# Kernel tuning notes

Hardware: AMD Instinct MI355X
Metric: run time of the kernel (lower is better)

The kernel has to match this reference:

```python
import jax, jax.numpy as jnp
import numpy as np

N = 100000
E = 1600000
IN_FEATS = 256
OUT_FEATS = 256
EPS_WSUM = 1e-8   # clamp for weight sum
EPS_NORM = 1e-12  # F.normalize eps


def setup_inputs() -> dict:
    key = jax.random.key(0)
    k1, k2, k3, k4, k5 = jax.random.split(key, 5)
    x = jax.random.normal(k1, (N, IN_FEATS), dtype=jnp.float32)
    edge_index = jax.random.randint(k2, (2, E), 0, N, dtype=jnp.int64)
    edge_weight = jax.random.uniform(k3, (E,), dtype=jnp.float32)
    # Xavier-uniform-like init scale for [out, in] weights
    lim = float(np.sqrt(6.0 / (IN_FEATS + OUT_FEATS)) * np.sqrt(2.0))
    W_self = jax.random.uniform(k4, (OUT_FEATS, IN_FEATS), dtype=jnp.float32, minval=-lim, maxval=lim)
    W_neigh = jax.random.uniform(k5, (OUT_FEATS, IN_FEATS), dtype=jnp.float32, minval=-lim, maxval=lim)
    bias = jnp.zeros((OUT_FEATS,), dtype=jnp.float32)
    return {"x": x, "edge_index": edge_index, "edge_weight": edge_weight,
            "W_self": W_self, "W_neigh": W_neigh, "bias": bias}


def reference(x, edge_index, edge_weight, W_self, W_neigh, bias):
    row, col = edge_index[0], edge_index[1]
    # weighted mean aggregation: gather -> scale -> scatter-add -> normalize by weight sum
    weighted = x[row] * edge_weight[:, None]                       # [E, in]
    num = jax.ops.segment_sum(weighted, col, num_segments=N)       # [N, in]
    wsum = jax.ops.segment_sum(edge_weight, col, num_segments=N)   # [N]
    wsum = jnp.maximum(wsum, EPS_WSUM)
    neigh = num / wsum[:, None]                                    # [N, in]
    out = x @ W_self.T + neigh @ W_neigh.T + bias                  # [N, out]
    # L2 normalize (torch F.normalize semantics)
    nrm = jnp.maximum(jnp.linalg.norm(out, axis=-1, keepdims=True), EPS_NORM)
    return out / nrm
```

## Files before the change

kernel.cpp:

```cpp
#include <hip/hip_runtime.h>
#include <hip/hip_bf16.h>
#include <stdint.h>

#define IN_F 256
#define K_TOT 512
#define GR 64

typedef __attribute__((ext_vector_type(8))) _Float16 f16x8;
typedef __attribute__((ext_vector_type(4))) _Float16 f16x4;
typedef __attribute__((ext_vector_type(4))) float f32x4;
typedef __attribute__((ext_vector_type(2))) float f32x2;

#if __has_builtin(__builtin_amdgcn_cvt_pk_f32_fp8) && __has_builtin(__builtin_amdgcn_cvt_pk_fp8_f32)
#define HW_FP8 1
#endif

__device__ __forceinline__ float fp8_dec1(uint32_t b) {
  union { uint16_t u; _Float16 h; } cv;
  cv.u = (uint16_t)((b & 0x7F) << 7);
  float v = (float)cv.h * 256.0f;
  return (b & 0x80) ? -v : v;
}
__device__ __forceinline__ uint32_t fp8_enc1(float f) {
  union { _Float16 h; uint16_t u; } cv;
  cv.h = (_Float16)(f * (1.0f / 256.0f));
  uint32_t s = (cv.u >> 8) & 0x80;
  uint32_t t = cv.u & 0x7FFF;
  uint32_t r = (t + 0x3F + ((t >> 7) & 1)) >> 7;
  if (r > 0x7E) r = 0x7E;
  return s | r;
}
__device__ __forceinline__ void fp8x4_dec(uint32_t w, float4& o) {
#ifdef HW_FP8
  f32x2 lo = __builtin_amdgcn_cvt_pk_f32_fp8((int)w, false);
  f32x2 hi = __builtin_amdgcn_cvt_pk_f32_fp8((int)w, true);
  o.x = lo[0]; o.y = lo[1]; o.z = hi[0]; o.w = hi[1];
#else
  o.x = fp8_dec1(w & 0xFF); o.y = fp8_dec1((w >> 8) & 0xFF);
  o.z = fp8_dec1((w >> 16) & 0xFF); o.w = fp8_dec1(w >> 24);
#endif
}
__device__ __forceinline__ uint32_t fp8x4_enc(float a, float b, float c, float d) {
#ifdef HW_FP8
  int r = __builtin_amdgcn_cvt_pk_fp8_f32(a, b, 0, false);
  r = __builtin_amdgcn_cvt_pk_fp8_f32(c, d, r, true);
  return (uint32_t)r;
#else
  return fp8_enc1(a) | (fp8_enc1(b) << 8) | (fp8_enc1(c) << 16) | (fp8_enc1(d) << 24);
#endif
}

__global__ void prep_kernel(const int* __restrict__ ei, int* __restrict__ counts,
                            int* __restrict__ flag, int N) {
  const int b = blockIdx.x;
  const int t = threadIdx.x;
  if (b == 0) {
    __shared__ int bad_s[256];
    int bad = 0;
#pragma unroll
    for (int p = 0; p < 8; ++p)
      if (ei[2 * (t + p * 256) + 1] != 0) bad = 1;
    bad_s[t] = bad;
    __syncthreads();
    for (int s = 128; s > 0; s >>= 1) {
      if (t < s) bad_s[t] |= bad_s[t + s];
      __syncthreads();
    }
    if (t == 0) *flag = (bad_s[0] == 0) ? 1 : 0;
  } else {
    int base = (b - 1) * 1024 + t * 4;
#pragma unroll
    for (int j = 0; j < 4; ++j)
      if (base + j < N) counts[base + j] = 0;
  }
}

__global__ void init_kernel(const float* __restrict__ x,
                            const float* __restrict__ Ws,
                            const float* __restrict__ Wn,
                            const int* __restrict__ ei,
                            _Float16* __restrict__ Bhi,
                            uint32_t* __restrict__ xq, _Float16* __restrict__ Af16,
                            int* __restrict__ counts, uint32_t* __restrict__ dstc,
                            const int* __restrict__ flag, int N, int E,
                            int nconv, int nhist) {
  const int b = blockIdx.x;
  const int t = threadIdx.x;
  if (b < 512) {
    int idx = b * 256 + t;
    int j = idx >> 9;
    int k = idx & 511;
    float v = (k < IN_F) ? Ws[j * IN_F + k] : Wn[j * IN_F + (k - IN_F)];
    size_t addr = ((size_t)(k >> 5) * 256 + j) * 32 + (k & 31);
    Bhi[addr] = (_Float16)v;
  } else {
    int m = b - 512;
    int npair = 2 * (nconv < nhist ? nconv : nhist);
    int role, ci;
    if (m < npair) { role = m & 1; ci = m >> 1; }
    else if (nconv > nhist) { role = 0; ci = nhist + (m - npair); }
    else { role = 1; ci = nconv + (m - npair); }
    if (role == 0) {
      size_t base = (size_t)ci * 4096 + (size_t)t * 16;
      size_t tot = (size_t)N * IN_F;
      if (base + 16 <= tot) {
        const float4* x4 = reinterpret_cast<const float4*>(x + base);
        float4 v0 = x4[0], v1 = x4[1], v2 = x4[2], v3 = x4[3];
        uint4 o;
        o.x = fp8x4_enc(v0.x, v0.y, v0.z, v0.w);
        o.y = fp8x4_enc(v1.x, v1.y, v1.z, v1.w);
        o.z = fp8x4_enc(v2.x, v2.y, v2.z, v2.w);
        o.w = fp8x4_enc(v3.x, v3.y, v3.z, v3.w);
        *reinterpret_cast<uint4*>(xq + base / 4) = o;
        size_t row = base >> 8;
        int col = (int)(base & 255);
        f16x8 h0 = {(_Float16)v0.x, (_Float16)v0.y, (_Float16)v0.z, (_Float16)v0.w,
                    (_Float16)v1.x, (_Float16)v1.y, (_Float16)v1.z, (_Float16)v1.w};
        f16x8 h1 = {(_Float16)v2.x, (_Float16)v2.y, (_Float16)v2.z, (_Float16)v2.w,
                    (_Float16)v3.x, (_Float16)v3.y, (_Float16)v3.z, (_Float16)v3.w};
        _Float16* dst = Af16 + row * K_TOT + col;
        *reinterpret_cast<f16x8*>(dst) = h0;
        *reinterpret_cast<f16x8*>(dst + 8) = h1;
      }
    } else {
      int is64 = *flag;
      int e = ci * 256 + t;
      if (e < E) {
        int dst = is64 ? ei[2 * (E + e)] : ei[E + e];
        int rank = atomicAdd(counts + dst, 1);
        dstc[e] = (uint32_t)dst | ((uint32_t)rank << 17);
      }
    }
  }
}

__global__ void scan1_kernel(const int* __restrict__ counts, int* __restrict__ offsets,
                             int* __restrict__ bsums, int N) {
  __shared__ int buf[1024];
  int t = threadIdx.x;
  int i = blockIdx.x * 1024 + t;
  int v = (i < N) ? counts[i] : 0;
  buf[t] = v;
  __syncthreads();
  for (int s = 1; s < 1024; s <<= 1) {
    int add = (t >= s) ? buf[t - s] : 0;
    __syncthreads();
    buf[t] += add;
    __syncthreads();
  }
  if (i < N) offsets[i] = buf[t] - v;
  if (t == 1023) bsums[blockIdx.x] = buf[1023];
}

__global__ void scan23_kernel(int* __restrict__ offsets, const int* __restrict__ bsums,
                              int N, int E, int nb) {
  __shared__ int sb[128];
  int t = threadIdx.x;
  int v = 0;
  if (t < 128) {
    v = (t < nb) ? bsums[t] : 0;
    sb[t] = v;
  }
  __syncthreads();
  for (int s = 1; s < 128; s <<= 1) {
    int add = 0;
    if (t < 128 && t >= s) add = sb[t - s];
    __syncthreads();
    if (t < 128) sb[t] += add;
    __syncthreads();
  }
  if (t < 128) sb[t] -= v;
  __syncthreads();
  int i = blockIdx.x * 256 + t;
  if (i < N) offsets[i] += sb[i >> 10];
  if (i == 0) offsets[N] = E;
}

__global__ void fill_kernel(const int* __restrict__ ei, const float* __restrict__ ew,
                            const uint32_t* __restrict__ dstc,
                            const int* __restrict__ offsets,
                            const int* __restrict__ flag,
                            uint32_t* __restrict__ edges, int E, int nper) {
  int q = blockIdx.x & 7;
  int e = (blockIdx.x >> 3) * 256 + threadIdx.x;
  if (e >= E) return;
  uint32_t dr = __builtin_nontemporal_load(dstc + e);
  int dst = (int)(dr & 0x1FFFFu);
  if ((unsigned)(dst - q * nper) >= (unsigned)nper) return;
  int rank = (int)(dr >> 17);
  int is64 = *flag;
  int src = is64 ? __builtin_nontemporal_load(ei + 2 * e)
                 : __builtin_nontemporal_load(ei + e);
  float w = __builtin_nontemporal_load(ew + e);
  uint32_t w15 = (uint32_t)__float2int_rn(w * 32767.0f);
  int pos = offsets[dst] + rank;
  edges[pos] = ((uint32_t)src << 15) | w15;
}

__launch_bounds__(256)
__global__ void aggregate_fp8_kernel(const uint8_t* __restrict__ xqb,
                                     const int* __restrict__ offsets,
                                     const uint32_t* __restrict__ edges,
                                     _Float16* __restrict__ Af16, int N) {
  int wid = blockIdx.x * 4 + (threadIdx.x >> 6);
  if (wid >= N) return;
  const uint32_t lane = threadIdx.x & 63;
  const uint32_t lane4 = lane * 4;
  int beg = offsets[wid];
  int end = offsets[wid + 1];
  float4 acc = {0.f, 0.f, 0.f, 0.f};
  float ws = 0.f;
  const float wscale = 1.0f / 32767.0f;
  int e = beg;
  for (; (e & 3) && e < end; ++e) {
    uint32_t n = edges[e];
    uint32_t qv = *reinterpret_cast<const uint32_t*>(xqb + ((n >> 7) & ~0xFFu) + lane4);
    float w0 = (float)(n & 0x7FFF) * wscale;
    float4 f;
    fp8x4_dec(qv, f);
    acc.x += f.x * w0; acc.y += f.y * w0; acc.z += f.z * w0; acc.w += f.w * w0;
    ws += w0;
  }
  for (; e + 7 < end; e += 8) {
    uint4 pa = *reinterpret_cast<const uint4*>(&edges[e]);
    uint4 pb = *reinterpret_cast<const uint4*>(&edges[e + 4]);
    uint32_t q0 = *reinterpret_cast<const uint32_t*>(xqb + ((pa.x >> 7) & ~0xFFu) + lane4);
    uint32_t q1 = *reinterpret_cast<const uint32_t*>(xqb + ((pa.y >> 7) & ~0xFFu) + lane4);
    uint32_t q2 = *reinterpret_cast<const uint32_t*>(xqb + ((pa.z >> 7) & ~0xFFu) + lane4);
    uint32_t q3 = *reinterpret_cast<const uint32_t*>(xqb + ((pa.w >> 7) & ~0xFFu) + lane4);
    uint32_t q4 = *reinterpret_cast<const uint32_t*>(xqb + ((pb.x >> 7) & ~0xFFu) + lane4);
    uint32_t q5 = *reinterpret_cast<const uint32_t*>(xqb + ((pb.y >> 7) & ~0xFFu) + lane4);
    uint32_t q6 = *reinterpret_cast<const uint32_t*>(xqb + ((pb.z >> 7) & ~0xFFu) + lane4);
    uint32_t q7 = *reinterpret_cast<const uint32_t*>(xqb + ((pb.w >> 7) & ~0xFFu) + lane4);
    float w0 = (float)(pa.x & 0x7FFF) * wscale, w1 = (float)(pa.y & 0x7FFF) * wscale;
    float w2 = (float)(pa.z & 0x7FFF) * wscale, w3 = (float)(pa.w & 0x7FFF) * wscale;
    float w4 = (float)(pb.x & 0x7FFF) * wscale, w5 = (float)(pb.y & 0x7FFF) * wscale;
    float w6 = (float)(pb.z & 0x7FFF) * wscale, w7 = (float)(pb.w & 0x7FFF) * wscale;
    float4 f0, f1, f2, f3, f4, f5, f6, f7;
    fp8x4_dec(q0, f0); fp8x4_dec(q1, f1); fp8x4_dec(q2, f2); fp8x4_dec(q3, f3);
    fp8x4_dec(q4, f4); fp8x4_dec(q5, f5); fp8x4_dec(q6, f6); fp8x4_dec(q7, f7);
    acc.x += f0.x * w0 + f1.x * w1 + f2.x * w2 + f3.x * w3 +
             f4.x * w4 + f5.x * w5 + f6.x * w6 + f7.x * w7;
    acc.y += f0.y * w0 + f1.y * w1 + f2.y * w2 + f3.y * w3 +
             f4.y * w4 + f5.y * w5 + f6.y * w6 + f7.y * w7;
    acc.z += f0.z * w0 + f1.z * w1 + f2.z * w2 + f3.z * w3 +
             f4.z * w4 + f5.z * w5 + f6.z * w6 + f7.z * w7;
    acc.w += f0.w * w0 + f1.w * w1 + f2.w * w2 + f3.w * w3 +
             f4.w * w4 + f5.w * w5 + f6.w * w6 + f7.w * w7;
    ws += w0 + w1 + w2 + w3 + w4 + w5 + w6 + w7;
  }
  for (; e + 3 < end; e += 4) {
    uint4 pa = *reinterpret_cast<const uint4*>(&edges[e]);
    uint32_t q0 = *reinterpret_cast<const uint32_t*>(xqb + ((pa.x >> 7) & ~0xFFu) + lane4);
    uint32_t q1 = *reinterpret_cast<const uint32_t*>(xqb + ((pa.y >> 7) & ~0xFFu) + lane4);
    uint32_t q2 = *reinterpret_cast<const uint32_t*>(xqb + ((pa.z >> 7) & ~0xFFu) + lane4);
    uint32_t q3 = *reinterpret_cast<const uint32_t*>(xqb + ((pa.w >> 7) & ~0xFFu) + lane4);
    float w0 = (float)(pa.x & 0x7FFF) * wscale, w1 = (float)(pa.y & 0x7FFF) * wscale;
    float w2 = (float)(pa.z & 0x7FFF) * wscale, w3 = (float)(pa.w & 0x7FFF) * wscale;
    float4 f0, f1, f2, f3;
    fp8x4_dec(q0, f0); fp8x4_dec(q1, f1); fp8x4_dec(q2, f2); fp8x4_dec(q3, f3);
    acc.x += f0.x * w0 + f1.x * w1 + f2.x * w2 + f3.x * w3;
    acc.y += f0.y * w0 + f1.y * w1 + f2.y * w2 + f3.y * w3;
    acc.z += f0.z * w0 + f1.z * w1 + f2.z * w2 + f3.z * w3;
    acc.w += f0.w * w0 + f1.w * w1 + f2.w * w2 + f3.w * w3;
    ws += w0 + w1 + w2 + w3;
  }
  for (; e < end; ++e) {
    uint32_t n = edges[e];
    uint32_t qv = *reinterpret_cast<const uint32_t*>(xqb + ((n >> 7) & ~0xFFu) + lane4);
    float w0 = (float)(n & 0x7FFF) * wscale;
    float4 f;
    fp8x4_dec(qv, f);
    acc.x += f.x * w0; acc.y += f.y * w0; acc.z += f.z * w0; acc.w += f.w * w0;
    ws += w0;
  }
  float inv = 1.f / fmaxf(ws, 1e-8f);
  f16x4 o = {(_Float16)(acc.x * inv), (_Float16)(acc.y * inv),
             (_Float16)(acc.z * inv), (_Float16)(acc.w * inv)};
  *reinterpret_cast<f16x4*>(Af16 + (size_t)wid * K_TOT + IN_F + lane4) = o;
}

__launch_bounds__(256)
__global__ void gemm_norm_kernel(const _Float16* __restrict__ Af16,
                                 const _Float16* __restrict__ Bhi,
                                 const float* __restrict__ bias,
                                 float* __restrict__ out, int N) {
  const int t = threadIdx.x;
  const int lane = t & 63;
  const int w = t >> 6;
  const int row0 = blockIdx.x * GR;

  __shared__ _Float16 Ah[2][256 * 8];
  __shared__ float ssb[GR][4];

  f32x4 acc[4][4];
#pragma unroll
  for (int rt = 0; rt < 4; ++rt)
#pragma unroll
    for (int ct = 0; ct < 4; ++ct) acc[rt][ct] = (f32x4){0.f, 0.f, 0.f, 0.f};

  int st_row = row0 + (t >> 6) * 16 + (t & 15);
  if (st_row >= N) st_row = N - 1;
  const _Float16* Abase = Af16 + (size_t)st_row * K_TOT + ((t >> 4) & 3) * 8;

  const size_t bfrag = (size_t)(w * 64 + (lane & 15)) * 32 + (lane >> 4) * 8;
  const _Float16* BhiP = Bhi + bfrag;

  *reinterpret_cast<f16x8*>(&Ah[0][t * 8]) = *reinterpret_cast<const f16x8*>(Abase);
  f16x8 a_next = *reinterpret_cast<const f16x8*>(Abase + 32);
  f16x8 bH[2][4];
#pragma unroll
  for (int ct = 0; ct < 4; ++ct) {
    bH[0][ct] = *reinterpret_cast<const f16x8*>(BhiP + ct * 512);
    bH[1][ct] = *reinterpret_cast<const f16x8*>(BhiP + 8192 + ct * 512);
  }
  __syncthreads();

#pragma unroll
  for (int ks = 0; ks < 16; ++ks) {
    f16x8 aH[4];
#pragma unroll
    for (int rt = 0; rt < 4; ++rt)
      aH[rt] = *reinterpret_cast<const f16x8*>(&Ah[ks & 1][(rt * 64 + lane) * 8]);
    f16x8 bNext[4];
    if (ks < 14) {
#pragma unroll
      for (int ct = 0; ct < 4; ++ct)
        bNext[ct] = *reinterpret_cast<const f16x8*>(BhiP + (size_t)(ks + 2) * 8192 + ct * 512);
    }
    if (ks < 15)
      *reinterpret_cast<f16x8*>(&Ah[(ks + 1) & 1][t * 8]) = a_next;
    if (ks < 14)
      a_next = *reinterpret_cast<const f16x8*>(Abase + (size_t)(ks + 2) * 32);
#pragma unroll
    for (int ct = 0; ct < 4; ++ct)
#pragma unroll
      for (int rt = 0; rt < 4; ++rt)
        acc[rt][ct] = __builtin_amdgcn_mfma_f32_16x16x32_f16(aH[rt], bH[ks & 1][ct], acc[rt][ct], 0, 0, 0);
    if (ks < 14) {
#pragma unroll
      for (int ct = 0; ct < 4; ++ct) bH[ks & 1][ct] = bNext[ct];
    }
    __syncthreads();
  }

  float bv[4];
#pragma unroll
  for (int ct = 0; ct < 4; ++ct) bv[ct] = bias[w * 64 + ct * 16 + (lane & 15)];

#pragma unroll
  for (int rt = 0; rt < 4; ++rt)
#pragma unroll
    for (int i = 0; i < 4; ++i) {
      float ssv = 0.f;
#pragma unroll
      for (int ct = 0; ct < 4; ++ct) {
        float val = acc[rt][ct][i] + bv[ct];
        acc[rt][ct][i] = val;
        ssv += val * val;
      }
#pragma unroll
      for (int s = 1; s < 16; s <<= 1) ssv += __shfl_xor(ssv, s, 64);
      if ((lane & 15) == 0) ssb[rt * 16 + (lane >> 4) * 4 + i][w] = ssv;
    }
  __syncthreads();

#pragma unroll
  for (int rt = 0; rt < 4; ++rt)
#pragma unroll
    for (int i = 0; i < 4; ++i) {
      int rl = rt * 16 + (lane >> 4) * 4 + i;
      f32x4 s4 = *reinterpret_cast<const f32x4*>(&ssb[rl][0]);
      float ss = s4[0] + s4[1] + s4[2] + s4[3];
      int gr = row0 + rl;
      if (gr < N) {
        float scale = 1.0f / fmaxf(sqrtf(ss), 1e-12f);
#pragma unroll
        for (int ct = 0; ct < 4; ++ct)
          out[(size_t)gr * IN_F + w * 64 + ct * 16 + (lane & 15)] = acc[rt][ct][i] * scale;
      }
    }
}

extern "C" void kernel_launch(void* const* d_in, const int* in_sizes, int n_in,
                              void* d_out, int out_size, void* d_ws, size_t ws_size,
                              hipStream_t stream) {
  const float* x = (const float*)d_in[0];
  const int* ei = (const int*)d_in[1];
  const float* ew = (const float*)d_in[2];
  const float* Wself = (const float*)d_in[3];
  const float* Wneigh = (const float*)d_in[4];
  const float* bias = (const float*)d_in[5];
  float* out = (float*)d_out;

  const int N = in_sizes[0] / IN_F;
  const int E = in_sizes[2];

  char* p = (char*)d_ws;
  _Float16* Af16 = (_Float16*)p;     p += (size_t)N * K_TOT * 2;
  _Float16* Bhi = (_Float16*)p;      p += (size_t)K_TOT * IN_F * 2;
  uint32_t* xq = (uint32_t*)p;       p += (size_t)N * IN_F;
  uint32_t* edges = (uint32_t*)p;    p += (size_t)E * 4;
  uint32_t* dstc = (uint32_t*)p;     p += (size_t)E * 4;
  int* counts = (int*)p;             p += (size_t)N * 4;
  int* offsets = (int*)p;            p += (size_t)(N + 1) * 4;
  int* bsums = (int*)p;              p += 128 * 4;
  int* flag = (int*)p;

  const int nconv = (int)(((size_t)N * IN_F + 4095) / 4096);
  const int nhist = (E + 255) / 256;
  const int nb = (N + 1023) / 1024;
  const int nper = (N + 7) / 8;
  const int nzero = (N + 1023) / 1024;

  prep_kernel<<<1 + nzero, 256, 0, stream>>>(ei, counts, flag, N);
  init_kernel<<<512 + nconv + nhist, 256, 0, stream>>>(
      x, Wself, Wneigh, ei, Bhi, xq, Af16, counts, dstc, flag, N, E, nconv, nhist);
  scan1_kernel<<<nb, 1024, 0, stream>>>(counts, offsets, bsums, N);
  scan23_kernel<<<(N + 255) / 256, 256, 0, stream>>>(offsets, bsums, N, E, nb);
  fill_kernel<<<((E + 255) / 256) * 8, 256, 0, stream>>>(ei, ew, dstc, offsets, flag,
                                                         edges, E, nper);
  aggregate_fp8_kernel<<<(N + 3) / 4, 256, 0, stream>>>(
      (const uint8_t*)xq, offsets, edges, Af16, N);
  gemm_norm_kernel<<<(N + GR - 1) / GR, 256, 0, stream>>>(Af16, Bhi, bias, out, N);
}
```

Before: 260.4 us.

## Store edge permutation instead of packed CSR payload; gather payload in aggregate

The histogram pass now writes a per-edge payload (source offset and full-precision weight) in original edge order, and the fill kernel only scatters the edge index into CSR order. The aggregation kernel reads that permutation and then does an extra indirect gather into the payload array before gathering features. This makes the fill scatter cheaper and keeps the weight at full fp32 instead of 15-bit, at the cost of an added dependent random 8-byte load per edge in the aggregation hot loop.

Result: slower. 278.7 us (+7.0%).

```diff
diff --git a/kernel.cpp b/kernel.cpp
--- a/kernel.cpp
+++ b/kernel.cpp
@@ -79,9 +79,11 @@
                             const float* __restrict__ Ws,
                             const float* __restrict__ Wn,
                             const int* __restrict__ ei,
+                            const float* __restrict__ ew,
                             _Float16* __restrict__ Bhi,
                             uint32_t* __restrict__ xq, _Float16* __restrict__ Af16,
                             int* __restrict__ counts, uint32_t* __restrict__ dstc,
+                            int2* __restrict__ pld,
                             const int* __restrict__ flag, int N, int E,
                             int nconv, int nhist) {
   const int b = blockIdx.x;
@@ -129,6 +131,8 @@
         int dst = is64 ? ei[2 * (E + e)] : ei[E + e];
         int rank = atomicAdd(counts + dst, 1);
         dstc[e] = (uint32_t)dst | ((uint32_t)rank << 17);
+        int src = is64 ? ei[2 * e] : ei[e];
+        pld[e] = make_int2(src << 8, __float_as_int(ew[e]));
       }
     }
   }
@@ -176,11 +180,9 @@
   if (i == 0) offsets[N] = E;
 }
 
-__global__ void fill_kernel(const int* __restrict__ ei, const float* __restrict__ ew,
-                            const uint32_t* __restrict__ dstc,
+__global__ void fill_kernel(const uint32_t* __restrict__ dstc,
                             const int* __restrict__ offsets,
-                            const int* __restrict__ flag,
-                            uint32_t* __restrict__ edges, int E, int nper) {
+                            uint32_t* __restrict__ perm, int E, int nper) {
   int q = blockIdx.x & 7;
   int e = (blockIdx.x >> 3) * 256 + threadIdx.x;
   if (e >= E) return;
@@ -188,54 +190,49 @@
   int dst = (int)(dr & 0x1FFFFu);
   if ((unsigned)(dst - q * nper) >= (unsigned)nper) return;
   int rank = (int)(dr >> 17);
-  int is64 = *flag;
-  int src = is64 ? __builtin_nontemporal_load(ei + 2 * e)
-                 : __builtin_nontemporal_load(ei + e);
-  float w = __builtin_nontemporal_load(ew + e);
-  uint32_t w15 = (uint32_t)__float2int_rn(w * 32767.0f);
-  int pos = offsets[dst] + rank;
-  edges[pos] = ((uint32_t)src << 15) | w15;
+  perm[offsets[dst] + rank] = (uint32_t)e;
 }
 
 __launch_bounds__(256)
 __global__ void aggregate_fp8_kernel(const uint8_t* __restrict__ xqb,
                                      const int* __restrict__ offsets,
-                                     const uint32_t* __restrict__ edges,
+                                     const uint32_t* __restrict__ perm,
+                                     const int2* __restrict__ pld,
                                      _Float16* __restrict__ Af16, int N) {
   int wid = blockIdx.x * 4 + (threadIdx.x >> 6);
   if (wid >= N) return;
-  const uint32_t lane = threadIdx.x & 63;
-  const uint32_t lane4 = lane * 4;
+  const uint32_t lane4 = (threadIdx.x & 63) * 4;
   int beg = offsets[wid];
   int end = offsets[wid + 1];
   float4 acc = {0.f, 0.f, 0.f, 0.f};
   float ws = 0.f;
-  const float wscale = 1.0f / 32767.0f;
   int e = beg;
   for (; (e & 3) && e < end; ++e) {
-    uint32_t n = edges[e];
-    uint32_t qv = *reinterpret_cast<const uint32_t*>(xqb + ((n >> 7) & ~0xFFu) + lane4);
-    float w0 = (float)(n & 0x7FFF) * wscale;
+    int2 l = pld[perm[e]];
+    uint32_t qv = *reinterpret_cast<const uint32_t*>(xqb + (uint32_t)l.x + lane4);
+    float w0 = __int_as_float(l.y);
     float4 f;
     fp8x4_dec(qv, f);
     acc.x += f.x * w0; acc.y += f.y * w0; acc.z += f.z * w0; acc.w += f.w * w0;
     ws += w0;
   }
   for (; e + 7 < end; e += 8) {
-    uint4 pa = *reinterpret_cast<const uint4*>(&edges[e]);
-    uint4 pb = *reinterpret_cast<const uint4*>(&edges[e + 4]);
-    uint32_t q0 = *reinterpret_cast<const uint32_t*>(xqb + ((pa.x >> 7) & ~0xFFu) + lane4);
-    uint32_t q1 = *reinterpret_cast<const uint32_t*>(xqb + ((pa.y >> 7) & ~0xFFu) + lane4);
-    uint32_t q2 = *reinterpret_cast<const uint32_t*>(xqb + ((pa.z >> 7) & ~0xFFu) + lane4);
-    uint32_t q3 = *reinterpret_cast<const uint32_t*>(xqb + ((pa.w >> 7) & ~0xFFu) + lane4);
-    uint32_t q4 = *reinterpret_cast<const uint32_t*>(xqb + ((pb.x >> 7) & ~0xFFu) + lane4);
-    uint32_t q5 = *reinterpret_cast<const uint32_t*>(xqb + ((pb.y >> 7) & ~0xFFu) + lane4);
-    uint32_t q6 = *reinterpret_cast<const uint32_t*>(xqb + ((pb.z >> 7) & ~0xFFu) + lane4);
-    uint32_t q7 = *reinterpret_cast<const uint32_t*>(xqb + ((pb.w >> 7) & ~0xFFu) + lane4);
-    float w0 = (float)(pa.x & 0x7FFF) * wscale, w1 = (float)(pa.y & 0x7FFF) * wscale;
-    float w2 = (float)(pa.z & 0x7FFF) * wscale, w3 = (float)(pa.w & 0x7FFF) * wscale;
-    float w4 = (float)(pb.x & 0x7FFF) * wscale, w5 = (float)(pb.y & 0x7FFF) * wscale;
-    float w6 = (float)(pb.z & 0x7FFF) * wscale, w7 = (float)(pb.w & 0x7FFF) * wscale;
+    uint4 pa = *reinterpret_cast<const uint4*>(&perm[e]);
+    uint4 pb = *reinterpret_cast<const uint4*>(&perm[e + 4]);
+    int2 l0 = pld[pa.x], l1 = pld[pa.y], l2 = pld[pa.z], l3 = pld[pa.w];
+    int2 l4 = pld[pb.x], l5 = pld[pb.y], l6 = pld[pb.z], l7 = pld[pb.w];
+    uint32_t q0 = *reinterpret_cast<const uint32_t*>(xqb + (uint32_t)l0.x + lane4);
+    uint32_t q1 = *reinterpret_cast<const uint32_t*>(xqb + (uint32_t)l1.x + lane4);
+    uint32_t q2 = *reinterpret_cast<const uint32_t*>(xqb + (uint32_t)l2.x + lane4);
+    uint32_t q3 = *reinterpret_cast<const uint32_t*>(xqb + (uint32_t)l3.x + lane4);
+    uint32_t q4 = *reinterpret_cast<const uint32_t*>(xqb + (uint32_t)l4.x + lane4);
+    uint32_t q5 = *reinterpret_cast<const uint32_t*>(xqb + (uint32_t)l5.x + lane4);
+    uint32_t q6 = *reinterpret_cast<const uint32_t*>(xqb + (uint32_t)l6.x + lane4);
+    uint32_t q7 = *reinterpret_cast<const uint32_t*>(xqb + (uint32_t)l7.x + lane4);
+    float w0 = __int_as_float(l0.y), w1 = __int_as_float(l1.y);
+    float w2 = __int_as_float(l2.y), w3 = __int_as_float(l3.y);
+    float w4 = __int_as_float(l4.y), w5 = __int_as_float(l5.y);
+    float w6 = __int_as_float(l6.y), w7 = __int_as_float(l7.y);
     float4 f0, f1, f2, f3, f4, f5, f6, f7;
     fp8x4_dec(q0, f0); fp8x4_dec(q1, f1); fp8x4_dec(q2, f2); fp8x4_dec(q3, f3);
     fp8x4_dec(q4, f4); fp8x4_dec(q5, f5); fp8x4_dec(q6, f6); fp8x4_dec(q7, f7);
@@ -250,13 +247,14 @@
     ws += w0 + w1 + w2 + w3 + w4 + w5 + w6 + w7;
   }
   for (; e + 3 < end; e += 4) {
-    uint4 pa = *reinterpret_cast<const uint4*>(&edges[e]);
-    uint32_t q0 = *reinterpret_cast<const uint32_t*>(xqb + ((pa.x >> 7) & ~0xFFu) + lane4);
-    uint32_t q1 = *reinterpret_cast<const uint32_t*>(xqb + ((pa.y >> 7) & ~0xFFu) + lane4);
-    uint32_t q2 = *reinterpret_cast<const uint32_t*>(xqb + ((pa.z >> 7) & ~0xFFu) + lane4);
-    uint32_t q3 = *reinterpret_cast<const uint32_t*>(xqb + ((pa.w >> 7) & ~0xFFu) + lane4);
-    float w0 = (float)(pa.x & 0x7FFF) * wscale, w1 = (float)(pa.y & 0x7FFF) * wscale;
-    float w2 = (float)(pa.z & 0x7FFF) * wscale, w3 = (float)(pa.w & 0x7FFF) * wscale;
+    uint4 pa = *reinterpret_cast<const uint4*>(&perm[e]);
+    int2 l0 = pld[pa.x], l1 = pld[pa.y], l2 = pld[pa.z], l3 = pld[pa.w];
+    uint32_t q0 = *reinterpret_cast<const uint32_t*>(xqb + (uint32_t)l0.x + lane4);
+    uint32_t q1 = *reinterpret_cast<const uint32_t*>(xqb + (uint32_t)l1.x + lane4);
+    uint32_t q2 = *reinterpret_cast<const uint32_t*>(xqb + (uint32_t)l2.x + lane4);
+    uint32_t q3 = *reinterpret_cast<const uint32_t*>(xqb + (uint32_t)l3.x + lane4);
+    float w0 = __int_as_float(l0.y), w1 = __int_as_float(l1.y);
+    float w2 = __int_as_float(l2.y), w3 = __int_as_float(l3.y);
     float4 f0, f1, f2, f3;
     fp8x4_dec(q0, f0); fp8x4_dec(q1, f1); fp8x4_dec(q2, f2); fp8x4_dec(q3, f3);
     acc.x += f0.x * w0 + f1.x * w1 + f2.x * w2 + f3.x * w3;
@@ -266,9 +264,9 @@
     ws += w0 + w1 + w2 + w3;
   }
   for (; e < end; ++e) {
-    uint32_t n = edges[e];
-    uint32_t qv = *reinterpret_cast<const uint32_t*>(xqb + ((n >> 7) & ~0xFFu) + lane4);
-    float w0 = (float)(n & 0x7FFF) * wscale;
+    int2 l = pld[perm[e]];
+    uint32_t qv = *reinterpret_cast<const uint32_t*>(xqb + (uint32_t)l.x + lane4);
+    float w0 = __int_as_float(l.y);
     float4 f;
     fp8x4_dec(qv, f);
     acc.x += f.x * w0; acc.y += f.y * w0; acc.z += f.z * w0; acc.w += f.w * w0;
@@ -400,7 +398,8 @@
   _Float16* Af16 = (_Float16*)p;     p += (size_t)N * K_TOT * 2;
   _Float16* Bhi = (_Float16*)p;      p += (size_t)K_TOT * IN_F * 2;
   uint32_t* xq = (uint32_t*)p;       p += (size_t)N * IN_F;
-  uint32_t* edges = (uint32_t*)p;    p += (size_t)E * 4;
+  uint32_t* perm = (uint32_t*)p;     p += (size_t)E * 4;
+  int2* pld = (int2*)p;              p += (size_t)E * 8;
   uint32_t* dstc = (uint32_t*)p;     p += (size_t)E * 4;
   int* counts = (int*)p;             p += (size_t)N * 4;
   int* offsets = (int*)p;            p += (size_t)(N + 1) * 4;
@@ -415,12 +414,12 @@
 
   prep_kernel<<<1 + nzero, 256, 0, stream>>>(ei, counts, flag, N);
   init_kernel<<<512 + nconv + nhist, 256, 0, stream>>>(
-      x, Wself, Wneigh, ei, Bhi, xq, Af16, counts, dstc, flag, N, E, nconv, nhist);
+      x, Wself, Wneigh, ei, ew, Bhi, xq, Af16, counts, dstc, pld, flag, N, E,
+      nconv, nhist);
   scan1_kernel<<<nb, 1024, 0, stream>>>(counts, offsets, bsums, N);
   scan23_kernel<<<(N + 255) / 256, 256, 0, stream>>>(offsets, bsums, N, E, nb);
-  fill_kernel<<<((E + 255) / 256) * 8, 256, 0, stream>>>(ei, ew, dstc, offsets, flag,
-                                                         edges, E, nper);
+  fill_kernel<<<((E + 255) / 256) * 8, 256, 0, stream>>>(dstc, offsets, perm, E, nper);
   aggregate_fp8_kernel<<<(N + 3) / 4, 256, 0, stream>>>(
-      (const uint8_t*)xq, offsets, edges, Af16, N);
+      (const uint8_t*)xq, offsets, perm, pld, Af16, N);
   gemm_norm_kernel<<<(N + GR - 1) / GR, 256, 0, stream>>>(Af16, Bhi, bias, out, N);
 }
```
